# Optimization experiments

Measured on AMD Instinct MI355X. Metric: run time of the kernel, lower is better.

## Reference

```python
import jax, jax.numpy as jnp
import numpy as np

N_GENES = 20000
UNITS = 10000
DEG = 32
BATCH = 128

def setup_inputs() -> dict:
    key = jax.random.key(0)
    k1, k2, k3, k4 = jax.random.split(key, 4)
    feature = jax.random.normal(k1, (BATCH, N_GENES), dtype=jnp.float32)
    ppi = jax.random.randint(k2, (UNITS, DEG), 0, N_GENES, dtype=jnp.int64)
    kernel = jax.random.normal(k3, (UNITS,), dtype=jnp.float32)
    bias = jax.random.normal(k4, (UNITS,), dtype=jnp.float32)
    return {"feature": feature, "ppi": ppi, "kernel": kernel, "bias": bias}

def reference(feature, ppi, kernel, bias):
    # gather along gene axis: [B, UNITS, DEG]
    h = jnp.abs(feature[:, ppi])
    # sum over neighbors -> [B, UNITS]
    h = jnp.sum(h, axis=-1)
    h = h * kernel + bias
    return jnp.tanh(h)
```

## Files before the change

### kernel.cpp

```cpp
#include <hip/hip_runtime.h>
#include <hip/hip_fp16.h>
#include <math.h>

#define N_GENES 20000
#define UNITS   10000
#define DEG     32
#define BATCH   128
#define UPB     16

__global__ __launch_bounds__(256) void transpose_abs_f16_kernel(
    const float* __restrict__ in, __half* __restrict__ out)
{
    __shared__ float tile[32][33];
    const int g0 = blockIdx.x * 32;
    const int b0 = blockIdx.y * 32;
    const int tx = threadIdx.x;
    const int ty = threadIdx.y;
#pragma unroll
    for (int i = 0; i < 32; i += 8)
        tile[ty + i][tx] = fabsf(in[(size_t)(b0 + ty + i) * N_GENES + (g0 + tx)]);
    __syncthreads();
#pragma unroll
    for (int i = 0; i < 32; i += 8)
        out[(size_t)(g0 + ty + i) * BATCH + (b0 + tx)] = __float2half(tile[tx][ty + i]);
}

__global__ __launch_bounds__(256) void gather_unit_kernel(
    const __half* __restrict__ featT,
    const int*   __restrict__ ppi,
    const float* __restrict__ kernelw,
    const float* __restrict__ bias,
    float*       __restrict__ out)
{
    __shared__ int   idx[UPB * DEG];
    __shared__ float res[UPB][BATCH];

    const int tid = threadIdx.x;
    const int u0  = blockIdx.x * UPB;

    {
        const int* src = ppi + (size_t)u0 * DEG;
        idx[tid]       = src[tid];
        idx[tid + 256] = src[tid + 256];
    }
    __syncthreads();

    const int lane = tid & 63;
    const int w    = tid >> 6;
    const int q    = lane >> 4;
    const int c    = lane & 15;

#pragma unroll 2
    for (int uu = 0; uu < 4; ++uu) {
        const int ul = w * 4 + uu;
        float acc[8] = {0.f,0.f,0.f,0.f,0.f,0.f,0.f,0.f};
#pragma unroll
        for (int it = 0; it < 8; ++it) {
            const int g = idx[ul * DEG + it * 4 + q];
            const float4 raw = *(const float4*)(featT + (size_t)g * BATCH + c * 8);
            const __half2* h2 = (const __half2*)&raw;
#pragma unroll
            for (int p = 0; p < 4; ++p) {
                const float2 f = __half22float2(h2[p]);
                acc[2 * p]     += f.x;
                acc[2 * p + 1] += f.y;
            }
        }
        const int u   = u0 + ul;
        const float kk = kernelw[u];
        const float bb = bias[u];
#pragma unroll
        for (int j = 0; j < 8; ++j) {
            float v = acc[j];
            v += __shfl_xor(v, 16, 64);
            v += __shfl_xor(v, 32, 64);
            acc[j] = v;
        }
        if (q == 0) {
#pragma unroll
            for (int j = 0; j < 8; ++j) {
                const float h = acc[j] * kk + bb;
                res[ul][c * 8 + j] = 1.f - 2.f / (__expf(2.f * h) + 1.f);
            }
        }
    }
    __syncthreads();

    const int b    = tid >> 1;
    const int half = tid & 1;
    float v[8];
#pragma unroll
    for (int j = 0; j < 8; ++j) v[j] = res[half * 8 + j][b];
    float4* o = (float4*)(out + (size_t)b * UNITS + u0 + half * 8);
    o[0] = make_float4(v[0], v[1], v[2], v[3]);
    o[1] = make_float4(v[4], v[5], v[6], v[7]);
}

extern "C" void kernel_launch(void* const* d_in, const int* in_sizes, int n_in,
                              void* d_out, int out_size, void* d_ws, size_t ws_size,
                              hipStream_t stream) {
    const float* feature = (const float*)d_in[0];
    const int*   ppi     = (const int*)d_in[1];
    const float* kernelw = (const float*)d_in[2];
    const float* bias    = (const float*)d_in[3];
    float* out   = (float*)d_out;
    __half* featT = (__half*)d_ws;

    dim3 g1(N_GENES / 32, BATCH / 32);
    dim3 b1(32, 8);
    transpose_abs_f16_kernel<<<g1, b1, 0, stream>>>(feature, featT);

    gather_unit_kernel<<<UNITS / UPB, 256, 0, stream>>>(
        featT, ppi, kernelw, bias, out);
}
```

Measured before the change: 80.60 us.

## Split transposed feature table into two 64-batch planes and gather half2 per lane

The transpose now writes the |feature| half table as two planes of 64 batch columns each, so each gene row in a plane is 128 bytes. The gather kernel loops over the planes, and each lane loads one half2 (4 bytes) per neighbour instead of a 16-byte float4, with two neighbours handled per wavefront step. The aim is to shrink the per-plane working set so it fits in cache better and to cut accumulator registers and shuffle reductions. The cost is twice as many gather iterations with narrower loads, and each index row is fetched once per plane.

```diff
diff --git a/kernel.cpp b/kernel.cpp
--- a/kernel.cpp
+++ b/kernel.cpp
@@ -20,9 +20,12 @@
     for (int i = 0; i < 32; i += 8)
         tile[ty + i][tx] = fabsf(in[(size_t)(b0 + ty + i) * N_GENES + (g0 + tx)]);
     __syncthreads();
+    const int b  = b0 + tx;
+    const size_t plane = (size_t)(b >> 6) * N_GENES * 64;
+    const int bp = b & 63;
 #pragma unroll
     for (int i = 0; i < 32; i += 8)
-        out[(size_t)(g0 + ty + i) * BATCH + (b0 + tx)] = __float2half(tile[tx][ty + i]);
+        out[plane + (size_t)(g0 + ty + i) * 64 + bp] = __float2half(tile[tx][ty + i]);
 }
 
 __global__ __launch_bounds__(256) void gather_unit_kernel(
@@ -47,40 +50,32 @@
 
     const int lane = tid & 63;
     const int w    = tid >> 6;
-    const int q    = lane >> 4;
-    const int c    = lane & 15;
+    const int c    = lane & 31;
+    const int dh   = lane >> 5;
 
+#pragma unroll
+    for (int p = 0; p < 2; ++p) {
+        const __half2* plane = (const __half2*)(featT + (size_t)p * N_GENES * 64);
 #pragma unroll 2
-    for (int uu = 0; uu < 4; ++uu) {
-        const int ul = w * 4 + uu;
-        float acc[8] = {0.f,0.f,0.f,0.f,0.f,0.f,0.f,0.f};
+        for (int uu = 0; uu < 4; ++uu) {
+            const int ul = w * 4 + uu;
+            float2 acc = {0.f, 0.f};
 #pragma unroll
-        for (int it = 0; it < 8; ++it) {
-            const int g = idx[ul * DEG + it * 4 + q];
-            const float4 raw = *(const float4*)(featT + (size_t)g * BATCH + c * 8);
-            const __half2* h2 = (const __half2*)&raw;
-#pragma unroll
-            for (int p = 0; p < 4; ++p) {
-                const float2 f = __half22float2(h2[p]);
-                acc[2 * p]     += f.x;
-                acc[2 * p + 1] += f.y;
+            for (int it = 0; it < 16; ++it) {
+                const int g = idx[ul * DEG + it * 2 + dh];
+                const float2 f = __half22float2(plane[(size_t)g * 32 + c]);
+                acc.x += f.x; acc.y += f.y;
             }
-        }
-        const int u   = u0 + ul;
-        const float kk = kernelw[u];
-        const float bb = bias[u];
-#pragma unroll
-        for (int j = 0; j < 8; ++j) {
-            float v = acc[j];
-            v += __shfl_xor(v, 16, 64);
-            v += __shfl_xor(v, 32, 64);
-            acc[j] = v;
-        }
-        if (q == 0) {
-#pragma unroll
-            for (int j = 0; j < 8; ++j) {
-                const float h = acc[j] * kk + bb;
-                res[ul][c * 8 + j] = 1.f - 2.f / (__expf(2.f * h) + 1.f);
+            acc.x += __shfl_xor(acc.x, 32, 64);
+            acc.y += __shfl_xor(acc.y, 32, 64);
+            if (dh == 0) {
+                const int u = u0 + ul;
+                const float kk = kernelw[u];
+                const float bb = bias[u];
+                const float h0 = acc.x * kk + bb;
+                const float h1 = acc.y * kk + bb;
+                res[ul][p * 64 + 2 * c]     = 1.f - 2.f / (__expf(2.f * h0) + 1.f);
+                res[ul][p * 64 + 2 * c + 1] = 1.f - 2.f / (__expf(2.f * h1) + 1.f);
             }
         }
     }
```

After: 80.05 us. About the same (-0.7%).
